# Kernel optimization log

Hardware: AMD Instinct MI355X
Metric: run time of the kernel (lower is better)

## Reference

```python
import jax, jax.numpy as jnp
import numpy as np

D_GNN = 256
K = 16
ATTN_DIM = 64
B = 65536
N_NODES = 100000
EPS = 1e-06


def setup_inputs() -> dict:
    key = jax.random.key(0)
    ks = jax.random.split(key, 8)
    center_emb = jax.random.normal(ks[0], (B, D_GNN), dtype=jnp.float32)
    all_embs = jax.random.normal(ks[1], (N_NODES, D_GNN), dtype=jnp.float32)
    neighbor_indices = jax.random.randint(ks[2], (B, K), 0, N_NODES, dtype=jnp.int64)
    neighbor_weights = jax.random.uniform(ks[3], (B, K), dtype=jnp.float32)
    # learned params (torch Linear weights, stored as [in, out] for x @ W)
    Wq = jax.random.normal(ks[4], (D_GNN, ATTN_DIM), dtype=jnp.float32) * 0.02
    Wk = jax.random.normal(ks[5], (D_GNN, ATTN_DIM), dtype=jnp.float32) * 0.02
    Wg = jax.random.normal(ks[6], (2 * D_GNN, D_GNN), dtype=jnp.float32) * 0.02
    bg = jnp.zeros((D_GNN,), dtype=jnp.float32)
    return {
        "center_emb": center_emb,
        "all_embs": all_embs,
        "neighbor_indices": neighbor_indices,
        "neighbor_weights": neighbor_weights,
        "Wq": Wq,
        "Wk": Wk,
        "Wg": Wg,
        "bg": bg,
    }


def reference(center_emb, all_embs, neighbor_indices, neighbor_weights, Wq, Wk, Wg, bg):
    scale = ATTN_DIM ** (-0.5)
    # gather K neighbor embeddings: [B, K, d]
    neigh_embs = all_embs[neighbor_indices]
    q = center_emb @ Wq                               # [B, A]
    k = jnp.einsum('bkd,da->bka', neigh_embs, Wk)     # [B, K, A]
    scores = jnp.einsum('ba,bka->bk', q, k) * scale   # [B, K]
    scores = scores + jnp.log(jnp.clip(neighbor_weights, EPS, None))
    pad_mask = neighbor_weights < EPS
    scores = jnp.where(pad_mask, -jnp.inf, scores)
    attn = jax.nn.softmax(scores, axis=-1)
    attn = jnp.nan_to_num(attn, nan=0.0)              # all-padded rows -> 0
    weighted_neigh = jnp.einsum('bk,bkd->bd', attn, neigh_embs)
    gate_in = jnp.concatenate([center_emb, weighted_neigh], axis=-1)
    gate = jax.nn.sigmoid(gate_in @ Wg + bg)
    return gate * center_emb + (1.0 - gate) * weighted_neigh
```

## Files before the change

### kernel.cpp

```cpp
#include <hip/hip_runtime.h>
#include <math.h>

#define D_GNN 256
#define ATTN  64
#define KNEI  16
#define NROWS 65536
#define NNODES 100000

constexpr float EPSV  = 1e-6f;
constexpr float SCALE = 0.125f;

typedef __attribute__((ext_vector_type(8))) short bf16x8;
typedef __attribute__((ext_vector_type(4))) float f32x4;

__device__ __forceinline__ unsigned short f2bf(float f) {
    union { float f; unsigned u; } v; v.f = f;
    return (unsigned short)((v.u + 0x7FFFu + ((v.u >> 16) & 1u)) >> 16);
}
__device__ __forceinline__ float bf2f(unsigned short h) {
    union { unsigned u; float f; } v; v.u = ((unsigned)h) << 16;
    return v.f;
}

typedef __attribute__((address_space(3))) short lds_short;
typedef __attribute__((address_space(1))) const short gm_short;
__device__ __forceinline__ void gload16(const unsigned short* g, short* l) {
    __builtin_amdgcn_global_load_lds((gm_short*)g, (lds_short*)l, 16, 0, 0);
}

__global__ __launch_bounds__(256) void conv_bf16(const float* __restrict__ in,
                                                 unsigned short* __restrict__ out) {
    size_t i = (size_t)blockIdx.x * 256 + threadIdx.x;
    float4 v = ((const float4*)in)[i];
    short4 o;
    o.x = (short)f2bf(v.x); o.y = (short)f2bf(v.y);
    o.z = (short)f2bf(v.z); o.w = (short)f2bf(v.w);
    ((short4*)out)[i] = o;
}

__global__ __launch_bounds__(256) void build_Mt(const float* __restrict__ Wq,
                                                const float* __restrict__ Wk,
                                                unsigned short* __restrict__ Mt) {
    __shared__ float wq[ATTN];
    int i = blockIdx.x;
    int j = threadIdx.x;
    if (j < ATTN) wq[j] = Wq[i * ATTN + j];
    __syncthreads();
    float s = 0.f;
#pragma unroll
    for (int a = 0; a < ATTN; ++a) s = fmaf(wq[a], Wk[j * ATTN + a], s);
    Mt[j * D_GNN + i] = f2bf(s);
}

__global__ __launch_bounds__(256) void conv_WgT(const float* __restrict__ Wg,
                                                unsigned short* __restrict__ WgT) {
    int k = blockIdx.x;
    int j = threadIdx.x;
    WgT[j * 512 + k] = f2bf(Wg[k * D_GNN + j]);
}

__global__ __launch_bounds__(256) void gemm_P_mfma(const unsigned short* __restrict__ Abf,
                                                   const unsigned short* __restrict__ Bt,
                                                   unsigned short* __restrict__ Pbf) {
    __shared__ short As[128 * 64];
    __shared__ short Bs[128 * 64];
    const int tid  = threadIdx.x;
    const int lane = tid & 63;
    const int wid  = tid >> 6;
    const int wr   = wid >> 1, wc = wid & 1;
    const int l15  = lane & 15, lg = lane >> 4;
    const int brow = blockIdx.x * 128;
    const int bcol = blockIdx.y * 128;

    f32x4 acc[4][4] = {};

    for (int k0 = 0; k0 < D_GNN; k0 += 64) {
#pragma unroll
        for (int is = 0; is < 4; ++is) {
            int off  = is * 4096 + tid * 16;
            int row  = off >> 7;
            int cs   = (off & 127) >> 1;
            int lofs = is * 2048 + wid * 512;
            gload16(Abf + (size_t)(brow + row) * D_GNN + k0 + cs, As + lofs);
            gload16(Bt  + (size_t)(bcol + row) * D_GNN + k0 + cs, Bs + lofs);
        }
        __syncthreads();
#pragma unroll
        for (int kk = 0; kk < 64; kk += 32) {
            bf16x8 af[4], bq[4];
#pragma unroll
            for (int m = 0; m < 4; ++m)
                af[m] = *(const bf16x8*)&As[(wr * 64 + m * 16 + l15) * 64 + kk + lg * 8];
#pragma unroll
            for (int n = 0; n < 4; ++n)
                bq[n] = *(const bf16x8*)&Bs[(wc * 64 + n * 16 + l15) * 64 + kk + lg * 8];
#pragma unroll
            for (int m = 0; m < 4; ++m)
#pragma unroll
                for (int n = 0; n < 4; ++n)
                    acc[m][n] = __builtin_amdgcn_mfma_f32_16x16x32_bf16(af[m], bq[n], acc[m][n], 0, 0, 0);
        }
        __syncthreads();
    }
#pragma unroll
    for (int m = 0; m < 4; ++m) {
        int row0 = brow + wr * 64 + m * 16 + lg * 4;
#pragma unroll
        for (int n = 0; n < 4; ++n) {
            int col = bcol + wc * 64 + n * 16 + l15;
#pragma unroll
            for (int r = 0; r < 4; ++r)
                Pbf[(size_t)(row0 + r) * D_GNN + col] = f2bf(acc[m][n][r]);
        }
    }
}

__global__ __launch_bounds__(256) void gather_attn(unsigned short* __restrict__ PW,
                                                   const unsigned short* __restrict__ allEbf,
                                                   const int* __restrict__ nidx,
                                                   const float* __restrict__ nw) {
    __shared__ short stage[4][KNEI * 512];

    int lane = threadIdx.x & 63;
    int wid  = threadIdx.x >> 6;
    int half = lane >> 5;
    int hl   = lane & 31;
    int b    = blockIdx.x * 8 + wid * 2 + half;

#pragma unroll
    for (int t = 0; t < KNEI; ++t) {
        int idx = nidx[b * KNEI + t];
        gload16(allEbf + (size_t)idx * D_GNN + hl * 8, &stage[wid][t * 512]);
    }

    bf16x8 pq = ((const bf16x8*)(PW + (size_t)b * D_GNN))[hl];
    float p[8];
#pragma unroll
    for (int j = 0; j < 8; ++j) p[j] = bf2f((unsigned short)pq[j]);

    __syncthreads();

    float sc[KNEI];
#pragma unroll
    for (int k = 0; k < KNEI; ++k) {
        bf16x8 v = *(const bf16x8*)&stage[wid][k * 512 + half * 256 + hl * 8];
        float s = 0.f;
#pragma unroll
        for (int j = 0; j < 8; ++j) s = fmaf(bf2f((unsigned short)v[j]), p[j], s);
        sc[k] = s;
    }

    float t8[8];
#pragma unroll
    for (int j = 0; j < 8; ++j) {
        float send = (hl & 16) ? sc[j] : sc[j + 8];
        float keep = (hl & 16) ? sc[j + 8] : sc[j];
        t8[j] = keep + __shfl_xor(send, 16);
    }
    float t4[4];
#pragma unroll
    for (int j = 0; j < 4; ++j) {
        float send = (hl & 1) ? t8[j] : t8[j + 4];
        float keep = (hl & 1) ? t8[j + 4] : t8[j];
        t4[j] = keep + __shfl_xor(send, 1);
    }
    float t2[2];
#pragma unroll
    for (int j = 0; j < 2; ++j) {
        float send = (hl & 2) ? t4[j] : t4[j + 2];
        float keep = (hl & 2) ? t4[j + 2] : t4[j];
        t2[j] = keep + __shfl_xor(send, 2);
    }
    float s1;
    {
        float send = (hl & 4) ? t2[0] : t2[1];
        float keep = (hl & 4) ? t2[1] : t2[0];
        s1 = keep + __shfl_xor(send, 4);
    }
    s1 += __shfl_xor(s1, 8);
    int kidx = ((hl >> 4) & 1) * 8 + (hl & 1) * 4 + ((hl >> 1) & 1) * 2 + ((hl >> 2) & 1);

    float w = nw[b * KNEI + kidx];
    float s = (w < EPSV) ? -INFINITY : fmaf(s1, SCALE, logf(w));

    float mx = s;
    mx = fmaxf(mx, __shfl_xor(mx, 16));
    mx = fmaxf(mx, __shfl_xor(mx, 1));
    mx = fmaxf(mx, __shfl_xor(mx, 2));
    mx = fmaxf(mx, __shfl_xor(mx, 4));
    float e = (mx > -INFINITY) ? expf(s - mx) : 0.f;
    float den = e;
    den += __shfl_xor(den, 16);
    den += __shfl_xor(den, 1);
    den += __shfl_xor(den, 2);
    den += __shfl_xor(den, 4);
    float a = (mx > -INFINITY) ? e / den : 0.f;

    float acc[8] = {};
#pragma unroll
    for (int k = 0; k < KNEI; ++k) {
        int sl = (((k >> 3) & 1) << 4) | ((k >> 2) & 1) | (((k >> 1) & 1) << 1) | ((k & 1) << 2);
        float ak = __shfl(a, sl, 32);
        bf16x8 v = *(const bf16x8*)&stage[wid][k * 512 + half * 256 + hl * 8];
#pragma unroll
        for (int j = 0; j < 8; ++j)
            acc[j] = fmaf(ak, bf2f((unsigned short)v[j]), acc[j]);
    }

    bf16x8 o;
#pragma unroll
    for (int j = 0; j < 8; ++j) o[j] = (short)f2bf(acc[j]);
    ((bf16x8*)(PW + (size_t)b * D_GNN))[hl] = o;
}

__global__ __launch_bounds__(256) void gate_gemm_mfma(const unsigned short* __restrict__ Cbf,
                                                      const unsigned short* __restrict__ Wbf,
                                                      const unsigned short* __restrict__ WgT,
                                                      const float* __restrict__ bg,
                                                      float* __restrict__ Out) {
    __shared__ short As[128 * 64];
    __shared__ short Bs[128 * 64];
    const int tid  = threadIdx.x;
    const int lane = tid & 63;
    const int wid  = tid >> 6;
    const int wr   = wid >> 1, wc = wid & 1;
    const int l15  = lane & 15, lg = lane >> 4;
    const int brow = blockIdx.x * 128;
    const int bcol = blockIdx.y * 128;

    f32x4 acc[4][4] = {};

    for (int k0 = 0; k0 < 2 * D_GNN; k0 += 64) {
        const unsigned short* Asrc = (k0 < D_GNN) ? Cbf : Wbf;
        int koff = k0 & (D_GNN - 1);
#pragma unroll
        for (int is = 0; is < 4; ++is) {
            int off  = is * 4096 + tid * 16;
            int row  = off >> 7;
            int cs   = (off & 127) >> 1;
            int lofs = is * 2048 + wid * 512;
            gload16(Asrc + (size_t)(brow + row) * D_GNN + koff + cs, As + lofs);
            gload16(WgT  + (size_t)(bcol + row) * 512 + k0 + cs,   Bs + lofs);
        }
        __syncthreads();
#pragma unroll
        for (int kk = 0; kk < 64; kk += 32) {
            bf16x8 af[4], bq[4];
#pragma unroll
            for (int m = 0; m < 4; ++m)
                af[m] = *(const bf16x8*)&As[(wr * 64 + m * 16 + l15) * 64 + kk + lg * 8];
#pragma unroll
            for (int n = 0; n < 4; ++n)
                bq[n] = *(const bf16x8*)&Bs[(wc * 64 + n * 16 + l15) * 64 + kk + lg * 8];
#pragma unroll
            for (int m = 0; m < 4; ++m)
#pragma unroll
                for (int n = 0; n < 4; ++n)
                    acc[m][n] = __builtin_amdgcn_mfma_f32_16x16x32_bf16(af[m], bq[n], acc[m][n], 0, 0, 0);
        }
        __syncthreads();
    }
#pragma unroll
    for (int m = 0; m < 4; ++m) {
        int row0 = brow + wr * 64 + m * 16 + lg * 4;
#pragma unroll
        for (int n = 0; n < 4; ++n) {
            int col = bcol + wc * 64 + n * 16 + l15;
            float bgc = bg[col];
#pragma unroll
            for (int r = 0; r < 4; ++r) {
                size_t rr = (size_t)(row0 + r);
                float g  = 1.f / (1.f + expf(-(acc[m][n][r] + bgc)));
                float cv = bf2f(Cbf[rr * D_GNN + col]);
                float wv = bf2f(Wbf[rr * D_GNN + col]);
                Out[rr * D_GNN + col] = fmaf(g, cv - wv, wv);
            }
        }
    }
}

extern "C" void kernel_launch(void* const* d_in, const int* in_sizes, int n_in,
                              void* d_out, int out_size, void* d_ws, size_t ws_size,
                              hipStream_t stream) {
    const float* center = (const float*)d_in[0];
    const float* allE   = (const float*)d_in[1];
    const int*   nidx   = (const int*)d_in[2];
    const float* nw     = (const float*)d_in[3];
    const float* Wq     = (const float*)d_in[4];
    const float* Wk     = (const float*)d_in[5];
    const float* Wg     = (const float*)d_in[6];
    const float* bg     = (const float*)d_in[7];
    float* out = (float*)d_out;

    unsigned short* Cbf    = (unsigned short*)d_ws;
    unsigned short* PW     = Cbf + (size_t)NROWS * D_GNN;
    unsigned short* allEbf = PW + (size_t)NROWS * D_GNN;
    unsigned short* Mt     = allEbf + (size_t)NNODES * D_GNN;
    unsigned short* WgT    = Mt + D_GNN * D_GNN;

    conv_bf16     <<<dim3(NROWS * D_GNN / 1024),  dim3(256), 0, stream>>>(center, Cbf);
    conv_bf16     <<<dim3(NNODES * D_GNN / 1024), dim3(256), 0, stream>>>(allE, allEbf);
    build_Mt      <<<dim3(D_GNN),                 dim3(256), 0, stream>>>(Wq, Wk, Mt);
    conv_WgT      <<<dim3(2 * D_GNN),             dim3(256), 0, stream>>>(Wg, WgT);
    gemm_P_mfma   <<<dim3(NROWS / 128, 2),        dim3(256), 0, stream>>>(Cbf, Mt, PW);
    gather_attn   <<<dim3(NROWS / 8),             dim3(256), 0, stream>>>(PW, allEbf, nidx, nw);
    gate_gemm_mfma<<<dim3(NROWS / 128, 2),        dim3(256), 0, stream>>>(Cbf, PW, WgT, bg, out);
}
```

Measured before the change: 209.5 us.

## Fuse center bf16 conversion into P GEMM and widen GEMM tiles to full width

```diff
diff --git a/kernel.cpp b/kernel.cpp
--- a/kernel.cpp
+++ b/kernel.cpp
@@ -59,45 +59,60 @@
     WgT[j * 512 + k] = f2bf(Wg[k * D_GNN + j]);
 }
 
-__global__ __launch_bounds__(256) void gemm_P_mfma(const unsigned short* __restrict__ Abf,
-                                                   const unsigned short* __restrict__ Bt,
-                                                   unsigned short* __restrict__ Pbf) {
+__global__ __launch_bounds__(256) void gemm_P_fused(const float* __restrict__ C32,
+                                                    const unsigned short* __restrict__ Mt,
+                                                    unsigned short* __restrict__ Cbf,
+                                                    unsigned short* __restrict__ Pbf) {
     __shared__ short As[128 * 64];
-    __shared__ short Bs[128 * 64];
+    __shared__ short Bs[256 * 64];
     const int tid  = threadIdx.x;
     const int lane = tid & 63;
     const int wid  = tid >> 6;
     const int wr   = wid >> 1, wc = wid & 1;
     const int l15  = lane & 15, lg = lane >> 4;
     const int brow = blockIdx.x * 128;
-    const int bcol = blockIdx.y * 128;
-
-    f32x4 acc[4][4] = {};
+
+    f32x4 acc[4][8] = {};
 
     for (int k0 = 0; k0 < D_GNN; k0 += 64) {
 #pragma unroll
-        for (int is = 0; is < 4; ++is) {
+        for (int is = 0; is < 8; ++is) {
             int off  = is * 4096 + tid * 16;
             int row  = off >> 7;
             int cs   = (off & 127) >> 1;
             int lofs = is * 2048 + wid * 512;
-            gload16(Abf + (size_t)(brow + row) * D_GNN + k0 + cs, As + lofs);
-            gload16(Bt  + (size_t)(bcol + row) * D_GNN + k0 + cs, Bs + lofs);
+            gload16(Mt + (size_t)row * D_GNN + k0 + cs, Bs + lofs);
+        }
+#pragma unroll
+        for (int is = 0; is < 4; ++is) {
+            int offsh = is * 2048 + tid * 8;
+            int row   = offsh >> 6;
+            int col   = offsh & 63;
+            size_t gp = (size_t)(brow + row) * D_GNN + k0 + col;
+            float4 v0 = *(const float4*)(C32 + gp);
+            float4 v1 = *(const float4*)(C32 + gp + 4);
+            bf16x8 h;
+            h[0] = (short)f2bf(v0.x); h[1] = (short)f2bf(v0.y);
+            h[2] = (short)f2bf(v0.z); h[3] = (short)f2bf(v0.w);
+            h[4] = (short)f2bf(v1.x); h[5] = (short)f2bf(v1.y);
+            h[6] = (short)f2bf(v1.z); h[7] = (short)f2bf(v1.w);
+            *(bf16x8*)&As[offsh] = h;
+            *(bf16x8*)(Cbf + gp) = h;
         }
         __syncthreads();
 #pragma unroll
         for (int kk = 0; kk < 64; kk += 32) {
-            bf16x8 af[4], bq[4];
+            bf16x8 af[4], bq[8];
 #pragma unroll
             for (int m = 0; m < 4; ++m)
                 af[m] = *(const bf16x8*)&As[(wr * 64 + m * 16 + l15) * 64 + kk + lg * 8];
 #pragma unroll
-            for (int n = 0; n < 4; ++n)
-                bq[n] = *(const bf16x8*)&Bs[(wc * 64 + n * 16 + l15) * 64 + kk + lg * 8];
+            for (int n = 0; n < 8; ++n)
+                bq[n] = *(const bf16x8*)&Bs[(wc * 128 + n * 16 + l15) * 64 + kk + lg * 8];
 #pragma unroll
             for (int m = 0; m < 4; ++m)
 #pragma unroll
-                for (int n = 0; n < 4; ++n)
+                for (int n = 0; n < 8; ++n)
                     acc[m][n] = __builtin_amdgcn_mfma_f32_16x16x32_bf16(af[m], bq[n], acc[m][n], 0, 0, 0);
         }
         __syncthreads();
@@ -106,8 +121,8 @@
     for (int m = 0; m < 4; ++m) {
         int row0 = brow + wr * 64 + m * 16 + lg * 4;
 #pragma unroll
-        for (int n = 0; n < 4; ++n) {
-            int col = bcol + wc * 64 + n * 16 + l15;
+        for (int n = 0; n < 8; ++n) {
+            int col = wc * 128 + n * 16 + l15;
 #pragma unroll
             for (int r = 0; r < 4; ++r)
                 Pbf[(size_t)(row0 + r) * D_GNN + col] = f2bf(acc[m][n][r]);
@@ -219,16 +234,15 @@
                                                       const float* __restrict__ bg,
                                                       float* __restrict__ Out) {
     __shared__ short As[128 * 64];
-    __shared__ short Bs[128 * 64];
+    __shared__ short Bs[256 * 64];
     const int tid  = threadIdx.x;
     const int lane = tid & 63;
     const int wid  = tid >> 6;
     const int wr   = wid >> 1, wc = wid & 1;
     const int l15  = lane & 15, lg = lane >> 4;
     const int brow = blockIdx.x * 128;
-    const int bcol = blockIdx.y * 128;
-
-    f32x4 acc[4][4] = {};
+
+    f32x4 acc[4][8] = {};
 
     for (int k0 = 0; k0 < 2 * D_GNN; k0 += 64) {
         const unsigned short* Asrc = (k0 < D_GNN) ? Cbf : Wbf;
@@ -240,22 +254,29 @@
             int cs   = (off & 127) >> 1;
             int lofs = is * 2048 + wid * 512;
             gload16(Asrc + (size_t)(brow + row) * D_GNN + koff + cs, As + lofs);
-            gload16(WgT  + (size_t)(bcol + row) * 512 + k0 + cs,   Bs + lofs);
+        }
+#pragma unroll
+        for (int is = 0; is < 8; ++is) {
+            int off  = is * 4096 + tid * 16;
+            int row  = off >> 7;
+            int cs   = (off & 127) >> 1;
+            int lofs = is * 2048 + wid * 512;
+            gload16(WgT + (size_t)row * 512 + k0 + cs, Bs + lofs);
         }
         __syncthreads();
 #pragma unroll
         for (int kk = 0; kk < 64; kk += 32) {
-            bf16x8 af[4], bq[4];
+            bf16x8 af[4], bq[8];
 #pragma unroll
             for (int m = 0; m < 4; ++m)
                 af[m] = *(const bf16x8*)&As[(wr * 64 + m * 16 + l15) * 64 + kk + lg * 8];
 #pragma unroll
-            for (int n = 0; n < 4; ++n)
-                bq[n] = *(const bf16x8*)&Bs[(wc * 64 + n * 16 + l15) * 64 + kk + lg * 8];
+            for (int n = 0; n < 8; ++n)
+                bq[n] = *(const bf16x8*)&Bs[(wc * 128 + n * 16 + l15) * 64 + kk + lg * 8];
 #pragma unroll
             for (int m = 0; m < 4; ++m)
 #pragma unroll
-                for (int n = 0; n < 4; ++n)
+                for (int n = 0; n < 8; ++n)
                     acc[m][n] = __builtin_amdgcn_mfma_f32_16x16x32_bf16(af[m], bq[n], acc[m][n], 0, 0, 0);
         }
         __syncthreads();
@@ -264,8 +285,8 @@
     for (int m = 0; m < 4; ++m) {
         int row0 = brow + wr * 64 + m * 16 + lg * 4;
 #pragma unroll
-        for (int n = 0; n < 4; ++n) {
-            int col = bcol + wc * 64 + n * 16 + l15;
+        for (int n = 0; n < 8; ++n) {
+            int col = wc * 128 + n * 16 + l15;
             float bgc = bg[col];
 #pragma unroll
             for (int r = 0; r < 4; ++r) {
@@ -298,11 +319,10 @@
     unsigned short* Mt     = allEbf + (size_t)NNODES * D_GNN;
     unsigned short* WgT    = Mt + D_GNN * D_GNN;
 
-    conv_bf16     <<<dim3(NROWS * D_GNN / 1024),  dim3(256), 0, stream>>>(center, Cbf);
     conv_bf16     <<<dim3(NNODES * D_GNN / 1024), dim3(256), 0, stream>>>(allE, allEbf);
     build_Mt      <<<dim3(D_GNN),                 dim3(256), 0, stream>>>(Wq, Wk, Mt);
     conv_WgT      <<<dim3(2 * D_GNN),             dim3(256), 0, stream>>>(Wg, WgT);
-    gemm_P_mfma   <<<dim3(NROWS / 128, 2),        dim3(256), 0, stream>>>(Cbf, Mt, PW);
+    gemm_P_fused  <<<dim3(NROWS / 128),           dim3(256), 0, stream>>>(center, Mt, Cbf, PW);
     gather_attn   <<<dim3(NROWS / 8),             dim3(256), 0, stream>>>(PW, allEbf, nidx, nw);
-    gate_gemm_mfma<<<dim3(NROWS / 128, 2),        dim3(256), 0, stream>>>(Cbf, PW, WgT, bg, out);
-}
+    gate_gemm_mfma<<<dim3(NROWS / 128),           dim3(256), 0, stream>>>(Cbf, PW, WgT, bg, out);
+}
```

Result: slower. 223.5 us (+6.7%).
